# Kernel tuning notes

Hardware: AMD Instinct MI355X
Metric: run time of the kernel (lower is better)

Reference implementation:

```python
import jax, jax.numpy as jnp
import numpy as np

B, T, C, Q, NW, MD = 4, 2048, 512, 300, 32, 256
WS, NC, S = 16, 4, 16
L = T - WS + 1  # unfold output length, stride 1, no pad


def _pe(x):
    # standard sinusoidal positional encoding added to x [B,t,d]
    t, d = x.shape[1], x.shape[2]
    pos = jnp.arange(t, dtype=jnp.float32)[:, None]
    div = jnp.exp(jnp.arange(0, d, 2, dtype=jnp.float32) * (-np.log(10000.0) / d))
    ang = pos * div                                   # [t, d//2]
    pe = jnp.stack([jnp.sin(ang), jnp.cos(ang)], axis=-1).reshape(t, d)
    return x + pe[None]


def _mlp(x, w1, b1, w2, b2):
    return jax.nn.relu(x @ w1 + b1) @ w2 + b2


def setup_inputs():
    key = jax.random.key(0)
    ks = iter(jax.random.split(key, 32))

    def lin(k, fin, fout):
        kw, kb = jax.random.split(k)
        return (jax.random.normal(kw, (fin, fout), jnp.float32) / np.sqrt(fin),
                jax.random.normal(kb, (fout,), jnp.float32) * 0.01)

    inp = {}
    inp["vis_feats"] = jax.random.normal(next(ks), (B, T, C), jnp.float32)
    inp["query_feats"] = jax.random.normal(next(ks), (B, NW, Q), jnp.float32)
    inp["vW1"], inp["vb1"] = lin(next(ks), C, C)
    inp["vW2"], inp["vb2"] = lin(next(ks), C, C)
    inp["s1W1"], inp["s1b1"] = lin(next(ks), Q, Q)
    inp["s1W2"], inp["s1b2"] = lin(next(ks), Q, C)
    inp["s2W1"], inp["s2b1"] = lin(next(ks), Q, Q)
    inp["s2W2"], inp["s2b2"] = lin(next(ks), Q, C)
    inp["pW1"], inp["pb1"] = lin(next(ks), NC * C, C)
    inp["pW2"], inp["pb2"] = lin(next(ks), C, 2)
    inp["mW"], inp["mb"] = lin(next(ks), C, MD)
    inp["stW"], inp["stb"] = lin(next(ks), MD * S, S)
    inp["enW"], inp["enb"] = lin(next(ks), MD * S, S)
    inp["vis_len"] = jax.random.randint(next(ks), (B,), L // 2, L + 1, dtype=jnp.int32)
    return inp


def reference(vis_feats, query_feats, vW1, vb1, vW2, vb2,
              s1W1, s1b1, s1W2, s1b2, s2W1, s2b1, s2W2, s2b2,
              pW1, pb1, pW2, pb2, mW, mb, stW, stb, enW, enb, vis_len):
    v = _mlp(_pe(vis_feats), vW1, vb1, vW2, vb2)                # [B,T,C]
    q = _pe(query_feats)
    enc1 = _mlp(q, s1W1, s1b1, s1W2, s1b2)                      # [B,NW,C]
    enc2 = _mlp(q, s2W1, s2b1, s2W2, s2b2)                      # [B,NW,C]
    sim = jnp.einsum('btc,bwc->btw', v, enc1)                   # [B,T,NW]

    widx = jnp.arange(L)[:, None] + jnp.arange(WS)[None, :]     # [L,WS] sliding windows
    vu = v[:, widx, :].reshape(B, L, NC, WS // NC, C).mean(axis=3)       # [B,L,NC,C] avg-pool per chunk
    bel = sim[:, widx, :].reshape(B, L, NC, WS // NC, NW).sum(axis=3)    # [B,L,NC,NW]
    labels = jnp.argmax(bel, axis=3)                            # [B,L,NC] selected word per chunk
    sel = jax.vmap(lambda e, lab: e[lab])(enc2, labels)         # [B,L,NC,C] gather word embeddings
    mod = sel * vu                                              # modulate

    pred = _mlp(mod.reshape(B, L, NC * C), pW1, pb1, pW2, pb2).transpose(0, 2, 1)  # [B,2,L]

    x = (mod @ mW + mb).reshape(B, L * NC, MD)                  # [B,N,MD]
    n = (vis_len * NC).astype(jnp.int32)                        # ragged valid length per batch
    i = jnp.arange(S, dtype=jnp.int32)
    starts = (n[:, None] * i[None, :]) // S                     # adaptive-maxpool bin bounds
    ends = (n[:, None] * (i[None, :] + 1) + S - 1) // S
    j = jnp.arange(L * NC, dtype=jnp.int32)
    cols = []
    for b in range(S):  # S is a small fixed constant (not a data dim)
        m = (j[None, :] >= starts[:, b:b + 1]) & (j[None, :] < ends[:, b:b + 1])  # [B,N]
        cols.append(jnp.max(jnp.where(m[:, :, None], x, -jnp.inf), axis=1))       # [B,MD]
    feat = jnp.stack(cols, axis=2).reshape(B, MD * S)           # [B,MD,S] flattened channel-major
    start = (feat @ stW + stb)[:, :, None]                      # [B,S,1]
    end = (feat @ enW + enb)[:, :, None]                        # [B,S,1]
    return pred, start, end
```

## Files before the change

kernel.cpp:

```cpp
#include <hip/hip_runtime.h>
#include <hip/hip_bf16.h>
#include <math.h>

#define BB 4
#define TT 2048
#define CC 512
#define QQ 300
#define NWW 32
#define MDD 256
#define WSS 16
#define NCC 4
#define SS 16
#define LL (TT - WSS + 1)
#define NSUB 8
#define PUL (TT - 3)

typedef __attribute__((ext_vector_type(8))) short short8;
typedef __attribute__((ext_vector_type(4))) short short4v;
typedef __attribute__((ext_vector_type(4))) float f32x4;

__device__ __forceinline__ void pe_add4(f32x4& v, int t, int gk0)
{
    #pragma unroll
    for (int j = 0; j < 4; j++) {
        int gk = gk0 + j;
        float di = expf((float)(gk & ~1) * (-9.210340371976184f / (float)CC));
        float ang = (float)t * di;
        v[j] += (gk & 1) ? cosf(ang) : sinf(ang);
    }
}

template<int PE>
__global__ __launch_bounds__(256, 2) void gemm_f32_fast(
    const float* __restrict__ A, const float* __restrict__ Bm,
    const float* __restrict__ bias, float* __restrict__ Cm,
    int M, int N, int K, int do_relu)
{
    __shared__ float As[2][32][68];
    __shared__ float Bs[2][32][128];
    const int bm = blockIdx.x * 64;
    const int bn = blockIdx.y * 128;
    const int tid = threadIdx.x;
    const int tx = tid & 31;
    const int ty = tid >> 5;

    float acc[8][4] = {};
    f32x4 pa[2], pb[4];
    int am[2], akq[2], bkr[4], bnq[4];
    #pragma unroll
    for (int i = 0; i < 2; i++) {
        int idx = i * 256 + tid;
        am[i] = idx >> 3; akq[i] = (idx & 7) * 4;
    }
    #pragma unroll
    for (int i = 0; i < 4; i++) {
        int idx = i * 256 + tid;
        bkr[i] = idx >> 5; bnq[i] = (idx & 31) * 4;
    }

    const int nk0 = K / 32;
    #pragma unroll
    for (int i = 0; i < 2; i++) {
        pa[i] = *(const f32x4*)(A + (size_t)(bm + am[i]) * K + akq[i]);
        if (PE) pe_add4(pa[i], (bm + am[i]) & (TT - 1), akq[i]);
    }
    #pragma unroll
    for (int i = 0; i < 4; i++)
        pb[i] = *(const f32x4*)(Bm + (size_t)bkr[i] * N + bn + bnq[i]);

    int buf = 0;
    for (int k0i = 0; ; k0i++) {
        #pragma unroll
        for (int i = 0; i < 2; i++)
            #pragma unroll
            for (int j = 0; j < 4; j++) As[buf][akq[i] + j][am[i]] = pa[i][j];
        #pragma unroll
        for (int i = 0; i < 4; i++)
            *(f32x4*)&Bs[buf][bkr[i]][bnq[i]] = pb[i];
        __syncthreads();
        if (k0i + 1 < nk0) {
            int k0 = (k0i + 1) * 32;
            #pragma unroll
            for (int i = 0; i < 2; i++) {
                pa[i] = *(const f32x4*)(A + (size_t)(bm + am[i]) * K + k0 + akq[i]);
                if (PE) pe_add4(pa[i], (bm + am[i]) & (TT - 1), k0 + akq[i]);
            }
            #pragma unroll
            for (int i = 0; i < 4; i++)
                pb[i] = *(const f32x4*)(Bm + (size_t)(k0 + bkr[i]) * N + bn + bnq[i]);
        }
        #pragma unroll 8
        for (int kk = 0; kk < 32; kk++) {
            f32x4 a0 = *(const f32x4*)&As[buf][kk][ty * 8];
            f32x4 a1 = *(const f32x4*)&As[buf][kk][ty * 8 + 4];
            f32x4 b0 = *(const f32x4*)&Bs[buf][kk][tx * 4];
            #pragma unroll
            for (int i2 = 0; i2 < 4; i2++)
                #pragma unroll
                for (int j2 = 0; j2 < 4; j2++) {
                    acc[i2][j2]     += a0[i2] * b0[j2];
                    acc[i2 + 4][j2] += a1[i2] * b0[j2];
                }
        }
        buf ^= 1;
        if (k0i + 1 == nk0) break;
    }

    #pragma unroll
    for (int i = 0; i < 8; i++) {
        int gm = bm + ty * 8 + i;
        f32x4 o;
        #pragma unroll
        for (int j = 0; j < 4; j++) {
            float v0 = acc[i][j] + bias[bn + tx * 4 + j];
            if (do_relu) v0 = fmaxf(v0, 0.f);
            o[j] = v0;
        }
        *(f32x4*)(Cm + (size_t)gm * N + bn + tx * 4) = o;
    }
}

__global__ void qpe_kernel(const float* __restrict__ q, float* __restrict__ out)
{
    int idx = blockIdx.x * 256 + threadIdx.x;
    if (idx >= BB * NWW * QQ) return;
    int qi = idx % QQ;
    int w  = (idx / QQ) % NWW;
    float di = expf((float)(qi & ~1) * (-9.210340371976184f / (float)QQ));
    float ang = (float)w * di;
    out[idx] = q[idx] + ((qi & 1) ? cosf(ang) : sinf(ang));
}

__global__ __launch_bounds__(64) void sgemm_dual2(
    const float* __restrict__ A1, const float* __restrict__ W1,
    const float* __restrict__ b1, float* __restrict__ C1,
    const float* __restrict__ A2, const float* __restrict__ W2,
    const float* __restrict__ b2, float* __restrict__ C2,
    int M, int N, int K, int do_relu)
{
    int id = blockIdx.x * 64 + threadIdx.x;
    if (id >= M * N) return;
    const float* A = blockIdx.y ? A2 : A1;
    const float* B = blockIdx.y ? W2 : W1;
    const float* bias = blockIdx.y ? b2 : b1;
    float* C = blockIdx.y ? C2 : C1;
    int m = id / N, n = id % N;
    const float* a = A + (size_t)m * K;
    const float* b = B + n;
    float acc = 0.f;
    int k = 0;
    for (; k + 10 <= K; k += 10) {
        float av[10], bv[10];
        #pragma unroll
        for (int u = 0; u < 10; u++) av[u] = a[k + u];
        #pragma unroll
        for (int u = 0; u < 10; u++) bv[u] = b[(size_t)(k + u) * N];
        #pragma unroll
        for (int u = 0; u < 10; u++) acc = fmaf(av[u], bv[u], acc);
    }
    for (; k < K; k++) acc = fmaf(a[k], b[(size_t)k * N], acc);
    float val = acc + bias[n];
    if (do_relu) val = fmaxf(val, 0.f);
    C[id] = val;
}

__global__ __launch_bounds__(256) void gemm_bf16_kernel(
    const short* __restrict__ A,
    const short* __restrict__ Bt,
    const float* __restrict__ bias, float* __restrict__ C,
    int M, int N, int K, int do_relu)
{
    __shared__ short As[128][40];
    __shared__ short Bs[128][40];
    const int bm = blockIdx.x * 128;
    const int bn = blockIdx.y * 128;
    const int tid = threadIdx.x;
    const int wave = tid >> 6, lane = tid & 63;
    const int wm = (wave & 1) * 64, wn = (wave >> 1) * 64;
    const int l15 = lane & 15, lk = (lane >> 4) * 8;
    const int srow = tid >> 2;
    const int scol = (tid & 3) * 8;

    f32x4 acc[4][4] = {};

    for (int k0 = 0; k0 < K; k0 += 32) {
        #pragma unroll
        for (int p = 0; p < 2; p++) {
            int row = p * 64 + srow;
            short8 av = {};
            int gm = bm + row;
            if (gm < M) av = *(const short8*)(A + (size_t)gm * K + k0 + scol);
            *(short8*)&As[row][scol] = av;
            short8 bv = {};
            int gn = bn + row;
            if (gn < N) bv = *(const short8*)(Bt + (size_t)gn * K + k0 + scol);
            *(short8*)&Bs[row][scol] = bv;
        }
        __syncthreads();

        short8 af[4], bf[4];
        #pragma unroll
        for (int mi = 0; mi < 4; mi++)
            af[mi] = *(const short8*)&As[wm + mi * 16 + l15][lk];
        #pragma unroll
        for (int ni = 0; ni < 4; ni++)
            bf[ni] = *(const short8*)&Bs[wn + ni * 16 + l15][lk];
        #pragma unroll
        for (int mi = 0; mi < 4; mi++)
            #pragma unroll
            for (int ni = 0; ni < 4; ni++)
                acc[mi][ni] = __builtin_amdgcn_mfma_f32_16x16x32_bf16(
                    af[mi], bf[ni], acc[mi][ni], 0, 0, 0);
        __syncthreads();
    }

    #pragma unroll
    for (int mi = 0; mi < 4; mi++) {
        int row0 = bm + wm + mi * 16 + (lane >> 4) * 4;
        #pragma unroll
        for (int ni = 0; ni < 4; ni++) {
            int col = bn + wn + ni * 16 + l15;
            float bsv = bias ? bias[col] : 0.f;
            #pragma unroll
            for (int r = 0; r < 4; r++) {
                int grow = row0 + r;
                if (grow >= M) continue;
                float val = acc[mi][ni][r] + bsv;
                if (do_relu) val = fmaxf(val, 0.f);
                C[(size_t)grow * N + col] = val;
            }
        }
    }
}

__global__ __launch_bounds__(256) void convT2_kernel(
    const float* __restrict__ src, __hip_bfloat16* __restrict__ dst,
    int K, int N)
{
    __shared__ float t[32][33];
    int c = threadIdx.x & 31, r4 = threadIdx.x >> 5;
    int n0 = blockIdx.x * 32, k0 = blockIdx.y * 32;
    #pragma unroll
    for (int rr = 0; rr < 32; rr += 8)
        t[rr + r4][c] = src[(size_t)(k0 + rr + r4) * N + n0 + c];
    __syncthreads();
    #pragma unroll
    for (int rr = 0; rr < 32; rr += 8)
        dst[(size_t)(n0 + rr + r4) * K + k0 + c] = __float2bfloat16(t[c][rr + r4]);
}

__global__ __launch_bounds__(256) void sim_kernel(
    const float* __restrict__ v, const float* __restrict__ enc1,
    float* __restrict__ sim)
{
    __shared__ float vs[8][CC];
    int blk = blockIdx.x;
    int b  = blk / (TT / 8);
    int t0 = (blk % (TT / 8)) * 8;
    int tid = threadIdx.x;
    for (int i = tid; i < 8 * (CC / 4); i += 256) {
        int r = i / (CC / 4), c = i % (CC / 4);
        *(f32x4*)&vs[r][c * 4] =
            *(const f32x4*)(v + ((size_t)b * TT + t0 + r) * CC + c * 4);
    }
    __syncthreads();
    int w  = tid & 31;
    int tt = tid >> 5;
    const f32x4* e4 = (const f32x4*)(enc1 + ((size_t)b * NWW + w) * CC);
    const f32x4* v4 = (const f32x4*)vs[tt];
    float s = 0.f;
    #pragma unroll 4
    for (int kq = 0; kq < CC / 4; kq++) {
        f32x4 vv = v4[kq], ee = e4[kq];
        s = fmaf(vv[0], ee[0], s);
        s = fmaf(vv[1], ee[1], s);
        s = fmaf(vv[2], ee[2], s);
        s = fmaf(vv[3], ee[3], s);
    }
    sim[((size_t)b * TT + t0 + tt) * NWW + w] = s;
}

__global__ __launch_bounds__(256) void pu_kernel(
    const float* __restrict__ v, float* __restrict__ pu)
{
    int idx = blockIdx.x * 256 + threadIdx.x;
    if (idx >= BB * PUL * (CC / 4)) return;
    int q = idx % (CC / 4);
    int t = (idx / (CC / 4)) % PUL;
    int b = idx / ((CC / 4) * PUL);
    const float* vp = v + ((size_t)b * TT + t) * CC + q * 4;
    f32x4 r0 = *(const f32x4*)vp;
    f32x4 r1 = *(const f32x4*)(vp + CC);
    f32x4 r2 = *(const f32x4*)(vp + 2 * CC);
    f32x4 r3 = *(const f32x4*)(vp + 3 * CC);
    f32x4 o;
    #pragma unroll
    for (int j = 0; j < 4; j++)
        o[j] = 0.25f * (((r0[j] + r1[j]) + r2[j]) + r3[j]);
    *(f32x4*)(pu + ((size_t)b * PUL + t) * CC + q * 4) = o;
}

__global__ __launch_bounds__(256) void mod_kernel(
    const float* __restrict__ pu, const float* __restrict__ sim,
    const float* __restrict__ enc2, __hip_bfloat16* __restrict__ modb)
{
    int blk = blockIdx.x;
    int b = blk / LL, l = blk % LL;
    int tid = threadIdx.x;
    int cch = tid >> 6;
    int lane = tid & 63;
    int t0 = l + cch * 4;

    int w = lane & 31;
    const float* sp = sim + ((size_t)b * TT + t0) * NWW + w;
    float bel = sp[0] + sp[NWW] + sp[2 * NWW] + sp[3 * NWW];
    int idx = w;
    #pragma unroll
    for (int m = 1; m < 32; m <<= 1) {
        float ov = __shfl_xor(bel, m);
        int   oi = __shfl_xor(idx, m);
        if (ov > bel || (ov == bel && oi < idx)) { bel = ov; idx = oi; }
    }

    const f32x4* e2 = (const f32x4*)(enc2 + ((size_t)b * NWW + idx) * CC);
    const f32x4* pq = (const f32x4*)(pu + ((size_t)b * PUL + t0) * CC);
    __hip_bfloat16* mp = modb + (((size_t)blk) * NCC + cch) * CC;
    #pragma unroll
    for (int q = lane; q < CC / 4; q += 64) {
        f32x4 e = e2[q], p = pq[q];
        short4v o;
        #pragma unroll
        for (int j = 0; j < 4; j++) {
            __hip_bfloat16 h = __float2bfloat16(e[j] * p[j]);
            o[j] = *(short*)&h;
        }
        *(short4v*)(mp + q * 4) = o;
    }
}

__global__ __launch_bounds__(256) void pred2w_kernel(
    const float* __restrict__ hpred, const float* __restrict__ pW2,
    const float* __restrict__ pb2, float* __restrict__ out)
{
    int row = blockIdx.x * 4 + (threadIdx.x >> 6);
    if (row >= BB * LL) return;
    int lane = threadIdx.x & 63;
    const float* h = hpred + (size_t)row * CC + lane * 8;
    f32x4 h0 = *(const f32x4*)h;
    f32x4 h1 = *(const f32x4*)(h + 4);
    const float* wp = pW2 + lane * 16;
    f32x4 w0 = *(const f32x4*)wp;
    f32x4 w1 = *(const f32x4*)(wp + 4);
    f32x4 w2 = *(const f32x4*)(wp + 8);
    f32x4 w3 = *(const f32x4*)(wp + 12);
    float s0 = h0[0]*w0[0] + h0[1]*w0[2] + h0[2]*w1[0] + h0[3]*w1[2]
             + h1[0]*w2[0] + h1[1]*w2[2] + h1[2]*w3[0] + h1[3]*w3[2];
    float s1 = h0[0]*w0[1] + h0[1]*w0[3] + h0[2]*w1[1] + h0[3]*w1[3]
             + h1[0]*w2[1] + h1[1]*w2[3] + h1[2]*w3[1] + h1[3]*w3[3];
    #pragma unroll
    for (int m = 32; m; m >>= 1) {
        s0 += __shfl_xor(s0, m);
        s1 += __shfl_xor(s1, m);
    }
    if (lane == 0) {
        int b = row / LL, l = row % LL;
        out[((size_t)b * 2 + 0) * LL + l] = s0 + pb2[0];
        out[((size_t)b * 2 + 1) * LL + l] = s1 + pb2[1];
    }
}

__global__ __launch_bounds__(256) void pool1_kernel(
    const float* __restrict__ x, const int* __restrict__ vis_len,
    float* __restrict__ scratch)
{
    int blk = blockIdx.x;
    int sub = blk % NSUB;
    int s   = (blk / NSUB) % SS;
    int b   = blk / (NSUB * SS);
    int n = vis_len[b] * NCC;
    int st = (n * s) / SS;
    int en = (n * (s + 1) + SS - 1) / SS;
    int len = en - st;
    int j0 = st + (len * sub) / NSUB;
    int j1 = st + (len * (sub + 1)) / NSUB;
    int md = threadIdx.x;
    float m = -INFINITY;
    const float* xp = x + (size_t)b * (LL * NCC) * MDD + md;
    for (int j = j0; j < j1; j++) m = fmaxf(m, xp[(size_t)j * MDD]);
    scratch[(size_t)blk * MDD + md] = m;
}

__global__ __launch_bounds__(256) void pool2_kernel(
    const float* __restrict__ scratch, float* __restrict__ feat)
{
    int blk = blockIdx.x;
    int md = threadIdx.x;
    const float* sp = scratch + (size_t)blk * NSUB * MDD + md;
    float m = sp[0];
    #pragma unroll
    for (int i = 1; i < NSUB; i++) m = fmaxf(m, sp[(size_t)i * MDD]);
    int b = blk / SS, s = blk % SS;
    feat[(size_t)b * MDD * SS + md * SS + s] = m;
}

__global__ void stend_kernel(const float* __restrict__ feat,
                             const float* __restrict__ stW, const float* __restrict__ stb,
                             const float* __restrict__ enW, const float* __restrict__ enb,
                             float* __restrict__ out)
{
    int bid = blockIdx.x;
    int which = bid >> 6;
    int r = bid & 63;
    int b = r >> 4, s = r & 15;
    int lane = threadIdx.x;
    const float* W  = which ? enW : stW;
    const float* bb = which ? enb : stb;
    const float* f  = feat + (size_t)b * MDD * SS;
    float acc = 0.f;
    for (int k = lane; k < MDD * SS; k += 64) acc += f[k] * W[(size_t)k * SS + s];
    #pragma unroll
    for (int m = 32; m; m >>= 1) acc += __shfl_xor(acc, m);
    if (lane == 0)
        out[(size_t)BB * 2 * LL + which * (BB * SS) + b * SS + s] = acc + bb[s];
}

extern "C" void kernel_launch(void* const* d_in, const int* in_sizes, int n_in,
                              void* d_out, int out_size, void* d_ws, size_t ws_size,
                              hipStream_t stream)
{
    const float* vis  = (const float*)d_in[0];
    const float* qf   = (const float*)d_in[1];
    const float* vW1  = (const float*)d_in[2];  const float* vb1 = (const float*)d_in[3];
    const float* vW2  = (const float*)d_in[4];  const float* vb2 = (const float*)d_in[5];
    const float* s1W1 = (const float*)d_in[6];  const float* s1b1= (const float*)d_in[7];
    const float* s1W2 = (const float*)d_in[8];  const float* s1b2= (const float*)d_in[9];
    const float* s2W1 = (const float*)d_in[10]; const float* s2b1= (const float*)d_in[11];
    const float* s2W2 = (const float*)d_in[12]; const float* s2b2= (const float*)d_in[13];
    const float* pW1  = (const float*)d_in[14]; const float* pb1 = (const float*)d_in[15];
    const float* pW2  = (const float*)d_in[16]; const float* pb2 = (const float*)d_in[17];
    const float* mW   = (const float*)d_in[18]; const float* mb  = (const float*)d_in[19];
    const float* stW  = (const float*)d_in[20]; const float* stb = (const float*)d_in[21];
    const float* enW  = (const float*)d_in[22]; const float* enb = (const float*)d_in[23];
    const int*   vlen = (const int*)d_in[24];
    float* out = (float*)d_out;

    float* ws   = (float*)d_ws;
    float* h1   = ws;
    float* v    = h1   + (size_t)BB * TT * CC;
    float* qpe  = v    + (size_t)BB * TT * CC;
    float* qh   = qpe  + (size_t)BB * NWW * QQ;
    float* enc1 = qh   + (size_t)BB * NWW * QQ;
    float* enc2 = enc1 + (size_t)BB * NWW * CC;
    float* sim  = enc2 + (size_t)BB * NWW * CC;
    float* feat = sim  + (size_t)BB * TT * NWW;
    float* x    = feat + (size_t)BB * MDD * SS;
    float* fend = x    + (size_t)BB * LL * NCC * MDD;
    __hip_bfloat16* modb = (__hip_bfloat16*)fend;
    __hip_bfloat16* pW1t = modb + (size_t)BB * LL * NCC * CC;
    __hip_bfloat16* mWt  = pW1t + (size_t)CC * (NCC * CC);
    float* qh2 = (float*)(mWt + (size_t)CC * MDD);

    const int MT = BB * TT;
    const int ML = BB * LL;
    const int MX = BB * LL * NCC;

    convT2_kernel<<<dim3(CC / 32, (NCC * CC) / 32), 256, 0, stream>>>(pW1, pW1t, NCC * CC, CC);
    convT2_kernel<<<dim3(MDD / 32, CC / 32), 256, 0, stream>>>(mW, mWt, CC, MDD);

    gemm_f32_fast<1><<<dim3(MT / 64, CC / 128), 256, 0, stream>>>(
        vis, vW1, vb1, h1, MT, CC, CC, 1);
    gemm_f32_fast<0><<<dim3(MT / 64, CC / 128), 256, 0, stream>>>(
        h1, vW2, vb2, v, MT, CC, CC, 0);
    qpe_kernel<<<(BB * NWW * QQ + 255) / 256, 256, 0, stream>>>(qf, qpe);
    sgemm_dual2<<<dim3((BB * NWW * QQ + 63) / 64, 2), 64, 0, stream>>>(
        qpe, s1W1, s1b1, qh, qpe, s2W1, s2b1, qh2, BB * NWW, QQ, QQ, 1);
    sgemm_dual2<<<dim3((BB * NWW * CC + 63) / 64, 2), 64, 0, stream>>>(
        qh, s1W2, s1b2, enc1, qh2, s2W2, s2b2, enc2, BB * NWW, CC, QQ, 0);
    sim_kernel<<<BB * (TT / 8), 256, 0, stream>>>(v, enc1, sim);
    pu_kernel<<<(BB * PUL * (CC / 4) + 255) / 256, 256, 0, stream>>>(v, h1);
    mod_kernel<<<BB * LL, 256, 0, stream>>>(h1, sim, enc2, modb);
    gemm_bf16_kernel<<<dim3((MX + 127) / 128, MDD / 128), 256, 0, stream>>>(
        (const short*)modb, (const short*)mWt, mb, x, MX, MDD, CC, 0);
    gemm_bf16_kernel<<<dim3((ML + 127) / 128, CC / 128), 256, 0, stream>>>(
        (const short*)modb, (const short*)pW1t, pb1, h1, ML, CC, NCC * CC, 1);
    pred2w_kernel<<<(ML + 3) / 4, 256, 0, stream>>>(h1, pW2, pb2, out);
    pool1_kernel<<<BB * SS * NSUB, 256, 0, stream>>>(x, vlen, sim);
    pool2_kernel<<<BB * SS, 256, 0, stream>>>(sim, feat);
    stend_kernel<<<128, 64, 0, stream>>>(feat, stW, stb, enW, enb, out);
}
```

Baseline: 408.4 us.

## Use K=64 bf16 GEMM tiles and split-K the pred hidden GEMM

Replaces the bf16 MFMA GEMM with a variant that stages 64-wide K slices per shared-memory load, halving the number of barrier-separated iterations. The pred-head GEMM (M≈8k, N=512, K=2048) now runs split-K over two z-slices that write partials into the x buffer, followed by a combine kernel that adds them with bias and ReLU. This raises block count for the low-occupancy GEMM, at the cost of extra partial-sum traffic and one more launch. The launches are reordered so x is reused as scratch before the mod GEMM overwrites it.

```diff
diff --git a/kernel.cpp b/kernel.cpp
--- a/kernel.cpp
+++ b/kernel.cpp
@@ -164,53 +164,61 @@
     C[id] = val;
 }
 
-__global__ __launch_bounds__(256) void gemm_bf16_kernel(
-    const short* __restrict__ A,
-    const short* __restrict__ Bt,
+template<int PARTIAL>
+__global__ __launch_bounds__(256) void gemm_bf16_k64(
+    const short* __restrict__ A, int lda,
+    const short* __restrict__ Bt, int ldb,
     const float* __restrict__ bias, float* __restrict__ C,
-    int M, int N, int K, int do_relu)
-{
-    __shared__ short As[128][40];
-    __shared__ short Bs[128][40];
+    int M, int N, int Kp, int do_relu)
+{
+    __shared__ short As[128][72];
+    __shared__ short Bs[128][72];
     const int bm = blockIdx.x * 128;
     const int bn = blockIdx.y * 128;
+    const int kbase = PARTIAL ? blockIdx.z * Kp : 0;
+    float* Cout = PARTIAL ? C + (size_t)blockIdx.z * ((size_t)M * N) : C;
     const int tid = threadIdx.x;
     const int wave = tid >> 6, lane = tid & 63;
     const int wm = (wave & 1) * 64, wn = (wave >> 1) * 64;
-    const int l15 = lane & 15, lk = (lane >> 4) * 8;
-    const int srow = tid >> 2;
-    const int scol = (tid & 3) * 8;
+    const int l15 = lane & 15;
+    const int lk0 = (lane >> 4) * 8;
+    const int srow = tid >> 3;
+    const int scol = (tid & 7) * 8;
 
     f32x4 acc[4][4] = {};
 
-    for (int k0 = 0; k0 < K; k0 += 32) {
-        #pragma unroll
-        for (int p = 0; p < 2; p++) {
-            int row = p * 64 + srow;
+    for (int k0 = kbase; k0 < kbase + Kp; k0 += 64) {
+        #pragma unroll
+        for (int p = 0; p < 4; p++) {
+            int row = p * 32 + srow;
             short8 av = {};
             int gm = bm + row;
-            if (gm < M) av = *(const short8*)(A + (size_t)gm * K + k0 + scol);
+            if (gm < M) av = *(const short8*)(A + (size_t)gm * lda + k0 + scol);
             *(short8*)&As[row][scol] = av;
             short8 bv = {};
             int gn = bn + row;
-            if (gn < N) bv = *(const short8*)(Bt + (size_t)gn * K + k0 + scol);
+            if (gn < N) bv = *(const short8*)(Bt + (size_t)gn * ldb + k0 + scol);
             *(short8*)&Bs[row][scol] = bv;
         }
         __syncthreads();
 
-        short8 af[4], bf[4];
-        #pragma unroll
-        for (int mi = 0; mi < 4; mi++)
-            af[mi] = *(const short8*)&As[wm + mi * 16 + l15][lk];
-        #pragma unroll
-        for (int ni = 0; ni < 4; ni++)
-            bf[ni] = *(const short8*)&Bs[wn + ni * 16 + l15][lk];
-        #pragma unroll
-        for (int mi = 0; mi < 4; mi++)
+        #pragma unroll
+        for (int ks = 0; ks < 2; ks++) {
+            int lk = lk0 + ks * 32;
+            short8 af[4], bf[4];
+            #pragma unroll
+            for (int mi = 0; mi < 4; mi++)
+                af[mi] = *(const short8*)&As[wm + mi * 16 + l15][lk];
             #pragma unroll
             for (int ni = 0; ni < 4; ni++)
-                acc[mi][ni] = __builtin_amdgcn_mfma_f32_16x16x32_bf16(
-                    af[mi], bf[ni], acc[mi][ni], 0, 0, 0);
+                bf[ni] = *(const short8*)&Bs[wn + ni * 16 + l15][lk];
+            #pragma unroll
+            for (int mi = 0; mi < 4; mi++)
+                #pragma unroll
+                for (int ni = 0; ni < 4; ni++)
+                    acc[mi][ni] = __builtin_amdgcn_mfma_f32_16x16x32_bf16(
+                        af[mi], bf[ni], acc[mi][ni], 0, 0, 0);
+        }
         __syncthreads();
     }
 
@@ -220,17 +228,28 @@
         #pragma unroll
         for (int ni = 0; ni < 4; ni++) {
             int col = bn + wn + ni * 16 + l15;
-            float bsv = bias ? bias[col] : 0.f;
+            float bsv = (!PARTIAL && bias) ? bias[col] : 0.f;
             #pragma unroll
             for (int r = 0; r < 4; r++) {
                 int grow = row0 + r;
                 if (grow >= M) continue;
                 float val = acc[mi][ni][r] + bsv;
-                if (do_relu) val = fmaxf(val, 0.f);
-                C[(size_t)grow * N + col] = val;
+                if (!PARTIAL && do_relu) val = fmaxf(val, 0.f);
+                Cout[(size_t)grow * N + col] = val;
             }
         }
     }
+}
+
+__global__ __launch_bounds__(256) void combine_kernel(
+    const float* __restrict__ p, const float* __restrict__ bias,
+    float* __restrict__ outh, int M, int N)
+{
+    int idx = blockIdx.x * 256 + threadIdx.x;
+    if (idx >= M * N) return;
+    int n = idx % N;
+    float v = p[idx] + p[(size_t)M * N + idx] + bias[n];
+    outh[idx] = fmaxf(v, 0.f);
 }
 
 __global__ __launch_bounds__(256) void convT2_kernel(
@@ -479,10 +498,13 @@
     sim_kernel<<<BB * (TT / 8), 256, 0, stream>>>(v, enc1, sim);
     pu_kernel<<<(BB * PUL * (CC / 4) + 255) / 256, 256, 0, stream>>>(v, h1);
     mod_kernel<<<BB * LL, 256, 0, stream>>>(h1, sim, enc2, modb);
-    gemm_bf16_kernel<<<dim3((MX + 127) / 128, MDD / 128), 256, 0, stream>>>(
-        (const short*)modb, (const short*)mWt, mb, x, MX, MDD, CC, 0);
-    gemm_bf16_kernel<<<dim3((ML + 127) / 128, CC / 128), 256, 0, stream>>>(
-        (const short*)modb, (const short*)pW1t, pb1, h1, ML, CC, NCC * CC, 1);
+    gemm_bf16_k64<1><<<dim3(ML / 128 + 1, CC / 128, 2), 256, 0, stream>>>(
+        (const short*)modb, NCC * CC, (const short*)pW1t, NCC * CC,
+        nullptr, x, ML, CC, (NCC * CC) / 2, 0);
+    combine_kernel<<<((size_t)ML * CC + 255) / 256, 256, 0, stream>>>(
+        x, pb1, h1, ML, CC);
+    gemm_bf16_k64<0><<<dim3((MX + 127) / 128, MDD / 128), 256, 0, stream>>>(
+        (const short*)modb, CC, (const short*)mWt, CC, mb, x, MX, MDD, CC, 0);
     pred2w_kernel<<<(ML + 3) / 4, 256, 0, stream>>>(h1, pW2, pb2, out);
     pool1_kernel<<<BB * SS * NSUB, 256, 0, stream>>>(x, vlen, sim);
     pool2_kernel<<<BB * SS, 256, 0, stream>>>(sim, feat);
```

New measurement: 397.2 us. 1.03x faster.
